# Kernel tuning notes

Measured on AMD Instinct MI355X. Metric: run time of the kernel, lower is better.

## Reference

```python
import jax, jax.numpy as jnp
import numpy as np

PATCH = 14
DIM = 512
LEVELS = 6
ITERS = LEVELS * 2  # default iters
TOKEN_ATTEND_SELF_VALUE = -0.0005


def setup_inputs() -> dict:
    key = jax.random.key(0)
    ks = jax.random.split(key, 9)
    b = 8
    # weights scaled down (~1/sqrt(dim)) so 12 iterations stay finite in fp32
    s = 0.02
    return {
        "img": jax.random.normal(ks[0], (b, 3, 224, 224), jnp.float32),
        "W_patch": jax.random.normal(ks[1], (PATCH * PATCH * 3, DIM), jnp.float32) * s,
        "b_patch": jax.random.normal(ks[2], (DIM,), jnp.float32) * s,
        "pos_emb": jax.random.normal(ks[3], (256, DIM), jnp.float32) * s,
        "init_levels": jax.random.normal(ks[4], (LEVELS, DIM), jnp.float32),
        "bu_in": jax.random.normal(ks[5], (LEVELS - 1, DIM, 4 * DIM), jnp.float32) * s,
        "bu_out": jax.random.normal(ks[6], (LEVELS - 1, 4 * DIM, DIM), jnp.float32) * s,
        "td_in": jax.random.normal(ks[7], (LEVELS - 1, DIM, 4 * DIM), jnp.float32) * s,
        "td_out": jax.random.normal(ks[8], (LEVELS - 1, 4 * DIM, DIM), jnp.float32) * s,
    }


def _grouped_ff(x, w_in, w_out):
    # x: [b, n, groups, d]; per-group two-layer FF with exact GELU
    h = jnp.einsum('bnld,lde->bnle', x, w_in)
    h = jax.nn.gelu(h, approximate=False)
    return jnp.einsum('bnld,lde->bnle', h, w_out)


def _consensus(levels):
    # levels: [b, n, l, d]; attend_self=False, no local radius
    n, d = levels.shape[1], levels.shape[-1]
    norm = jnp.maximum(jnp.linalg.norm(levels, axis=-1, keepdims=True), 1e-12)
    k = levels / norm
    sim = jnp.einsum('bild,bjld->blij', levels, k) * (d ** -0.5)
    eye = jnp.eye(n, dtype=bool)[None, None]
    sim = jnp.where(eye, jnp.asarray(TOKEN_ATTEND_SELF_VALUE, sim.dtype), sim)
    attn = jax.nn.softmax(sim, axis=-1)
    return jnp.einsum('blij,bjld->bild', attn, levels)


def reference(img, W_patch, b_patch, pos_emb, init_levels, bu_in, bu_out, td_in, td_out):
    b, c, H, W = img.shape
    p = PATCH
    h, w = H // p, W // p
    # 'b c (h p1) (w p2) -> b (h w) (p1 p2 c)'
    x = img.reshape(b, c, h, p, w, p).transpose(0, 2, 4, 3, 5, 1).reshape(b, h * w, p * p * c)
    tokens = x @ W_patch + b_patch  # [b, n, d]
    n = tokens.shape[1]
    pos = pos_emb[:n][None, :, None, :]       # [1, n, 1, d]
    bottom = tokens[:, :, None, :]            # [b, n, 1, d]
    levels = jnp.broadcast_to(init_levels[None, None], (b, n, LEVELS, DIM))

    for _ in range(ITERS):
        lwi = jnp.concatenate([bottom, levels], axis=2)            # [b, n, L+1, d]
        bu = _grouped_ff(lwi[:, :, 1:-1], bu_in, bu_out)           # [b, n, L-1, d]
        td = _grouped_ff(lwi[:, :, 2:] + pos, td_in, td_out)       # [b, n, L-1, d]
        bu = jnp.concatenate([bottom, bu], axis=2)                 # [b, n, L, d]
        td = jnp.pad(td, ((0, 0), (0, 0), (0, 1), (0, 0)))         # [b, n, L, d]
        cons = _consensus(levels)
        levels = (levels + bu + td + cons) * 0.25
    return levels
```

## Files before the change

### kernel.cpp

```cpp
#include <hip/hip_runtime.h>
#include <hip/hip_bf16.h>
#include <math.h>

#define B_   8
#define N_   256
#define L_   6
#define D_   512
#define NT_  2048
#define HID_ 2048

typedef __attribute__((ext_vector_type(4))) float f32x4;
typedef __attribute__((ext_vector_type(8))) short bf16x8;

struct bf16x4s { __hip_bfloat16 x, y, z, w; };

__device__ __forceinline__ bf16x4s to_bf4(float a, float b, float c, float d) {
    bf16x4s r;
    r.x = __float2bfloat16(a); r.y = __float2bfloat16(b);
    r.z = __float2bfloat16(c); r.w = __float2bfloat16(d);
    return r;
}

__device__ __forceinline__ void gload16(const void* g, void* l) {
    __builtin_amdgcn_global_load_lds(
        (const __attribute__((address_space(1))) int*)g,
        (__attribute__((address_space(3))) int*)l, 16, 0, 0);
}

template<int BM, int BN, int WM, int WN, typename CT, bool GELU>
__global__ __launch_bounds__(512, 4) void gemm_ff(
    const __hip_bfloat16* __restrict__ A1, int lda1, long az1,
    const __hip_bfloat16* __restrict__ A2, int lda2, long az2, int zsplit,
    const __hip_bfloat16* __restrict__ B, int ldb, long bz,
    CT* __restrict__ C, int ldc, long cz, int K)
{
    constexpr int WVM = BM / WM, WVN = BN / WN;
    constexpr int MR = WVM / 16, NR = WVN / 16;
    constexpr int ALOADS = (BM * 64) / (512 * 8);
    constexpr int BLOADS = (BN * 64) / (512 * 8);
    constexpr int LOADS  = ALOADS + BLOADS;

    __shared__ short As[2][BM * 64];
    __shared__ short Bs[2][BN * 64];

    const int tid = threadIdx.x;
    const int wv = tid >> 6, lane = tid & 63;
    const int wr = wv / WN, wc = wv % WN;

    const int gx = gridDim.x, gy = gridDim.y;
    const int nwg = gx * gy * gridDim.z;
    int lid = (blockIdx.z * gy + blockIdx.y) * gx + blockIdx.x;
    lid = (lid & 7) * (nwg >> 3) + (lid >> 3);
    const int bx = lid % gx, by = (lid / gx) % gy, bzz = lid / (gx * gy);

    const __hip_bfloat16* A;
    int lda;
    if (bzz < zsplit) { A = A1 + (long)bzz * az1;            lda = lda1; }
    else              { A = A2 + (long)(bzz - zsplit) * az2; lda = lda2; }
    B += (long)bzz * bz;  C += (long)bzz * cz;
    const int m0 = by * BM, n0 = bx * BN;

    f32x4 acc[MR][NR] = {};

    const int srow_a = tid >> 3, sslot = tid & 7;

#define STAGE(BUF, K0)                                                        \
    {                                                                         \
        _Pragma("unroll")                                                     \
        for (int i = 0; i < ALOADS; ++i) {                                    \
            const int row = srow_a + i * 64;                                  \
            const int gs  = sslot ^ (row & 7);                                \
            gload16(A + (long)(m0 + row) * lda + (K0) + gs * 8,               \
                    &As[BUF][(wv * 64 + i * 512) * 8]);                       \
        }                                                                     \
        _Pragma("unroll")                                                     \
        for (int i = 0; i < BLOADS; ++i) {                                    \
            const int row = srow_a + i * 64;                                  \
            const int gs  = sslot ^ (row & 7);                                \
            gload16(B + (long)(n0 + row) * ldb + (K0) + gs * 8,               \
                    &Bs[BUF][(wv * 64 + i * 512) * 8]);                       \
        }                                                                     \
    }

    const int fr = lane & 15, k4 = lane >> 4;
    const int nt = K / 64;
    int cur = 0;

    STAGE(0, 0);

    for (int t = 0; t < nt; ++t) {
        if (t + 1 < nt) {
            STAGE(cur ^ 1, (t + 1) * 64);
            asm volatile("s_waitcnt vmcnt(%0)\n\ts_barrier"
                         :: "n"(LOADS) : "memory");
        } else {
            asm volatile("s_waitcnt vmcnt(0)\n\ts_barrier" ::: "memory");
        }

#pragma unroll
        for (int ks = 0; ks < 2; ++ks) {
            bf16x8 af[MR], bf[NR];
#pragma unroll
            for (int i = 0; i < MR; ++i) {
                const int r = wr * WVM + i * 16 + fr;
                af[i] = *(const bf16x8*)&As[cur][r * 64 + ((ks * 4 + k4) ^ (r & 7)) * 8];
            }
#pragma unroll
            for (int j = 0; j < NR; ++j) {
                const int r = wc * WVN + j * 16 + fr;
                bf[j] = *(const bf16x8*)&Bs[cur][r * 64 + ((ks * 4 + k4) ^ (r & 7)) * 8];
            }
            __builtin_amdgcn_s_setprio(1);
#pragma unroll
            for (int i = 0; i < MR; ++i)
#pragma unroll
                for (int j = 0; j < NR; ++j)
                    acc[i][j] = __builtin_amdgcn_mfma_f32_16x16x32_bf16(
                        af[i], bf[j], acc[i][j], 0, 0, 0);
            __builtin_amdgcn_s_setprio(0);
        }
        asm volatile("s_waitcnt lgkmcnt(0)\n\ts_barrier" ::: "memory");
        cur ^= 1;
    }
#undef STAGE

    const int cr4 = (lane >> 4) * 4, cc = lane & 15;
#pragma unroll
    for (int i = 0; i < MR; ++i)
#pragma unroll
        for (int j = 0; j < NR; ++j) {
            const int col = n0 + wc * WVN + j * 16 + cc;
#pragma unroll
            for (int r = 0; r < 4; ++r) {
                const int row = m0 + wr * WVM + i * 16 + cr4 + r;
                float v = acc[i][j][r];
                if (GELU) v = 0.5f * v * (1.0f + erff(v * 0.70710678118654752f));
                CT* p = &C[(long)row * ldc + col];
                if constexpr (sizeof(CT) == 2) *p = __float2bfloat16(v);
                else *p = (CT)v;
            }
        }
}

__device__ __forceinline__ void mfma_kloop(
    const __hip_bfloat16* __restrict__ A, int lda,
    const __hip_bfloat16* __restrict__ B, int ldb,
    int m0, int n0, int K, short* As, short* Bs,
    f32x4 acc[4][4], int wave, int lane)
{
    const int srow_in = lane >> 2;
    const int sslot   = lane & 3;
    const int wm = (wave >> 1) * 64, wn = (wave & 1) * 64;

    for (int k0 = 0; k0 < K; k0 += 32) {
        __syncthreads();
#pragma unroll
        for (int c = 0; c < 2; ++c) {
            const int rbase = c * 64 + wave * 16;
            const int row   = rbase + srow_in;
            const int gk    = sslot ^ ((row >> 1) & 3);
            gload16(A + (long)(m0 + row) * lda + k0 + gk * 8, As + rbase * 32);
            gload16(B + (long)(n0 + row) * ldb + k0 + gk * 8, Bs + rbase * 32);
        }
        __syncthreads();

        const int fr = lane & 15, ksub = lane >> 4;
        bf16x8 af[4], bfr[4];
#pragma unroll
        for (int i = 0; i < 4; ++i) {
            const int ra = wm + i * 16 + fr;
            af[i]  = *(const bf16x8*)(As + ra * 32 + (ksub ^ ((ra >> 1) & 3)) * 8);
            const int rb = wn + i * 16 + fr;
            bfr[i] = *(const bf16x8*)(Bs + rb * 32 + (ksub ^ ((rb >> 1) & 3)) * 8);
        }
#pragma unroll
        for (int i = 0; i < 4; ++i)
#pragma unroll
            for (int j = 0; j < 4; ++j)
                acc[i][j] = __builtin_amdgcn_mfma_f32_16x16x32_bf16(
                    af[i], bfr[j], acc[i][j], 0, 0, 0);
    }
}

template<typename CT, bool GELU>
__global__ __launch_bounds__(256) void gemm_mfma(
    const __hip_bfloat16* __restrict__ A, int lda, long az,
    const __hip_bfloat16* __restrict__ B, int ldb, long bz,
    CT* __restrict__ C, int ldc, long cz, int K,
    const float* __restrict__ bias)
{
    __shared__ short As[128 * 32];
    __shared__ short Bs[128 * 32];
    const int tid = threadIdx.x;
    const int wave = tid >> 6, lane = tid & 63;
    const int z = blockIdx.z;
    A += (long)z * az;  B += (long)z * bz;  C += (long)z * cz;
    const int m0 = blockIdx.y * 128, n0 = blockIdx.x * 128;
    const int wm = (wave >> 1) * 64, wn = (wave & 1) * 64;

    f32x4 acc[4][4] = {};
    mfma_kloop(A, lda, B, ldb, m0, n0, K, As, Bs, acc, wave, lane);

    const int cr = lane >> 4, cc = lane & 15;
#pragma unroll
    for (int j = 0; j < 4; ++j) {
        const int col = n0 + wn + j * 16 + cc;
        const float bv = bias ? bias[col] : 0.f;
#pragma unroll
        for (int i = 0; i < 4; ++i)
#pragma unroll
            for (int r = 0; r < 4; ++r) {
                const int row = m0 + wm + i * 16 + cr * 4 + r;
                float v = acc[i][j][r] + bv;
                if (GELU) v = 0.5f * v * (1.0f + erff(v * 0.70710678118654752f));
                CT* p = &C[(long)row * ldc + col];
                if constexpr (sizeof(CT) == 2) *p = __float2bfloat16(v);
                else *p = (CT)v;
            }
    }
}

__global__ __launch_bounds__(256) void sim_mfma(
    const __hip_bfloat16* __restrict__ lev_bf, const float* __restrict__ invn,
    float* __restrict__ sim)
{
    __shared__ short As[128 * 32];
    __shared__ short Bs[128 * 32];
    const int tid = threadIdx.x;
    const int wave = tid >> 6, lane = tid & 63;
    const int z = blockIdx.z;
    const int b = z / 6, l = z - 6 * b;
    const __hip_bfloat16* base = lev_bf + (long)b * (N_ * L_ * D_) + (long)l * D_;
    const int m0 = blockIdx.y * 128, n0 = blockIdx.x * 128;
    const int wm = (wave >> 1) * 64, wn = (wave & 1) * 64;

    f32x4 acc[4][4] = {};
    mfma_kloop(base, L_ * D_, base, L_ * D_, m0, n0, D_, As, Bs, acc, wave, lane);

    const int cr = lane >> 4, cc = lane & 15;
    const float sc = 0.044194173824159216f;
#pragma unroll
    for (int j = 0; j < 4; ++j) {
        const int jg = n0 + wn + j * 16 + cc;
        const float iv = invn[((long)b * N_ + jg) * L_ + l] * sc;
#pragma unroll
        for (int i = 0; i < 4; ++i)
#pragma unroll
            for (int r = 0; r < 4; ++r) {
                const int ig = m0 + wm + i * 16 + cr * 4 + r;
                float v = acc[i][j][r] * iv;
                if (ig == jg) v = -0.0005f;
                sim[((long)z * N_ + ig) * N_ + jg] = v;
            }
    }
}

__global__ __launch_bounds__(256) void cons_mfma(
    const __hip_bfloat16* __restrict__ attn, const __hip_bfloat16* __restrict__ levT,
    float* __restrict__ cons)
{
    __shared__ short As[128 * 32];
    __shared__ short Bs[128 * 32];
    const int tid = threadIdx.x;
    const int wave = tid >> 6, lane = tid & 63;
    const int z = blockIdx.z;
    const int b = z / 6, l = z - 6 * b;
    const __hip_bfloat16* A = attn + (long)z * N_ * N_;
    const __hip_bfloat16* B = levT + (long)z * D_ * N_;
    float* C = cons + (long)b * (N_ * L_ * D_) + (long)l * D_;
    const int m0 = blockIdx.y * 128, n0 = blockIdx.x * 128;
    const int wm = (wave >> 1) * 64, wn = (wave & 1) * 64;

    f32x4 acc[4][4] = {};
    mfma_kloop(A, N_, B, N_, m0, n0, N_, As, Bs, acc, wave, lane);

    const int cr = lane >> 4, cc = lane & 15;
#pragma unroll
    for (int j = 0; j < 4; ++j) {
        const int col = n0 + wn + j * 16 + cc;
#pragma unroll
        for (int i = 0; i < 4; ++i)
#pragma unroll
            for (int r = 0; r < 4; ++r) {
                const int row = m0 + wm + i * 16 + cr * 4 + r;
                C[(long)row * (L_ * D_) + col] = acc[i][j][r];
            }
    }
}

__global__ __launch_bounds__(256) void transpose_to_bf16(
    const float* __restrict__ src, __hip_bfloat16* __restrict__ dst,
    int R, int Cc)
{
    __shared__ float t[32][33];
    const int zz = blockIdx.z;
    src += (long)zz * R * Cc;  dst += (long)zz * R * Cc;
    const int tx = threadIdx.x & 31, ty = threadIdx.x >> 5;
    const int c0 = blockIdx.x * 32, r0 = blockIdx.y * 32;
#pragma unroll
    for (int i = 0; i < 4; ++i)
        t[ty + i * 8][tx] = src[(long)(r0 + ty + i * 8) * Cc + c0 + tx];
    __syncthreads();
#pragma unroll
    for (int i = 0; i < 4; ++i)
        dst[(long)(c0 + ty + i * 8) * R + r0 + tx] = __float2bfloat16(t[tx][ty + i * 8]);
}

__global__ __launch_bounds__(256) void levT_kernel(
    const float* __restrict__ levels, __hip_bfloat16* __restrict__ levT)
{
    __shared__ float t[32][33];
    const int z = blockIdx.z;
    const int b = z / 6, l = z - 6 * b;
    const float* base = levels + (long)b * (N_ * L_ * D_) + (long)l * D_;
    const int tx = threadIdx.x & 31, ty = threadIdx.x >> 5;
    const int d0 = blockIdx.x * 32, j0 = blockIdx.y * 32;
#pragma unroll
    for (int i = 0; i < 4; ++i)
        t[ty + i * 8][tx] = base[(long)(j0 + ty + i * 8) * (L_ * D_) + d0 + tx];
    __syncthreads();
#pragma unroll
    for (int i = 0; i < 4; ++i)
        levT[(long)z * D_ * N_ + (long)(d0 + ty + i * 8) * N_ + j0 + tx] =
            __float2bfloat16(t[tx][ty + i * 8]);
}

__global__ __launch_bounds__(256) void invnorm_kernel(
    const float* __restrict__ levels, float* __restrict__ invn)
{
    const int wid = blockIdx.x * 4 + (threadIdx.x >> 6);
    const int lane = threadIdx.x & 63;
    const float* row = levels + (long)wid * 512;
    float s = 0.f;
#pragma unroll
    for (int k = lane * 4; k < 512; k += 256) {
        const float4 v = *(const float4*)&row[k];
        s += v.x * v.x + v.y * v.y + v.z * v.z + v.w * v.w;
    }
#pragma unroll
    for (int o = 1; o < 64; o <<= 1) s += __shfl_xor(s, o);
    if (lane == 0) invn[wid] = 1.0f / fmaxf(sqrtf(s), 1e-12f);
}

__global__ __launch_bounds__(256) void softmax_kernel(
    const float* __restrict__ sim, __hip_bfloat16* __restrict__ attn)
{
    const long row = (long)blockIdx.x * 4 + (threadIdx.x >> 6);
    const int lane = threadIdx.x & 63;
    const float* p = sim + row * 256;
    float4 v = *(const float4*)&p[lane * 4];
    float m = fmaxf(fmaxf(v.x, v.y), fmaxf(v.z, v.w));
#pragma unroll
    for (int o = 1; o < 64; o <<= 1) m = fmaxf(m, __shfl_xor(m, o));
    v.x = expf(v.x - m); v.y = expf(v.y - m);
    v.z = expf(v.z - m); v.w = expf(v.w - m);
    float s = v.x + v.y + v.z + v.w;
#pragma unroll
    for (int o = 1; o < 64; o <<= 1) s += __shfl_xor(s, o);
    const float inv = 1.0f / s;
    *(bf16x4s*)&attn[row * 256 + lane * 4] =
        to_bf4(v.x * inv, v.y * inv, v.z * inv, v.w * inv);
}

__global__ __launch_bounds__(256) void patchify_kernel(
    const float* __restrict__ img, __hip_bfloat16* __restrict__ Xp)
{
    const int t = blockIdx.x;
    const int b = t >> 8, n = t & 255;
    const int hh = n >> 4, ww = n & 15;
    for (int k = threadIdx.x; k < 608; k += 256) {
        float v = 0.f;
        if (k < 588) {
            const int c = k % 3;
            const int pj = (k / 3) % 14;
            const int pi = k / 42;
            v = img[(((long)b * 3 + c) * 224 + (hh * 14 + pi)) * 224 + (ww * 14 + pj)];
        }
        Xp[(long)t * 608 + k] = __float2bfloat16(v);
    }
}

__global__ __launch_bounds__(256) void wpT_kernel(
    const float* __restrict__ Wp, __hip_bfloat16* __restrict__ WpT)
{
    __shared__ float t[32][33];
    const int k0 = blockIdx.x * 32, d0 = blockIdx.y * 32;
    const int tx = threadIdx.x & 31, ty = threadIdx.x >> 5;
#pragma unroll
    for (int i = 0; i < 4; ++i) {
        const int k = k0 + ty + i * 8;
        t[ty + i * 8][tx] = (k < 588) ? Wp[(long)k * 512 + d0 + tx] : 0.f;
    }
    __syncthreads();
#pragma unroll
    for (int i = 0; i < 4; ++i)
        WpT[(long)(d0 + ty + i * 8) * 608 + k0 + tx] = __float2bfloat16(t[tx][ty + i * 8]);
}

__global__ __launch_bounds__(256) void init_levels_kernel(
    float* __restrict__ levels, const float* __restrict__ initlv)
{
    const long f = (long)blockIdx.x * 256 + threadIdx.x;
    const int d4 = f & 127;
    const int l = (int)((f >> 7) % 6);
    *(float4*)&levels[f * 4] = *(const float4*)&initlv[(long)l * 512 + d4 * 4];
}

__global__ __launch_bounds__(256) void lev_lp_init(
    const float* __restrict__ levels, const float* __restrict__ pos,
    __hip_bfloat16* __restrict__ lev_bf, __hip_bfloat16* __restrict__ lp_bf)
{
    const long f = (long)blockIdx.x * 256 + threadIdx.x;
    const int d4 = f & 127;
    const long tl = f >> 7;
    const int l = (int)(tl % 6);
    const long t = tl / 6;
    const float4 v = *(const float4*)&levels[f * 4];
    *(bf16x4s*)&lev_bf[f * 4] = to_bf4(v.x, v.y, v.z, v.w);
    if (l >= 1) {
        const float4 p = *(const float4*)&pos[(long)(t & 255) * 512 + d4 * 4];
        *(bf16x4s*)&lp_bf[((t * 5 + l - 1) * 512) + d4 * 4] =
            to_bf4(v.x + p.x, v.y + p.y, v.z + p.z, v.w + p.w);
    }
}

__global__ __launch_bounds__(256) void update_kernel(
    float* __restrict__ levels, const float* __restrict__ tokens,
    const float* __restrict__ acc_bu, const float* __restrict__ acc_td,
    const float* __restrict__ cons, const float* __restrict__ pos,
    __hip_bfloat16* __restrict__ lev_bf, __hip_bfloat16* __restrict__ lp_bf,
    float* __restrict__ invn)
{
    const int wid = blockIdx.x * 4 + (threadIdx.x >> 6);
    const int lane = threadIdx.x & 63;
    const int l = wid % 6;
    const long t = wid / 6;
    const long rowoff = (long)wid * 512;

    float ss = 0.f;
#pragma unroll
    for (int half = 0; half < 2; ++half) {
        const int k = lane * 4 + half * 256;
        const long off = rowoff + k;
        float4 lev = *(const float4*)&levels[off];
        const float4 cns = *(const float4*)&cons[off];
        float4 ac;
        if (l == 0) ac = *(const float4*)&tokens[t * 512 + k];
        else        ac = *(const float4*)&acc_bu[((long)(l - 1) * NT_ + t) * 512 + k];
        if (l < 5) {
            const float4 td = *(const float4*)&acc_td[((long)l * NT_ + t) * 512 + k];
            ac.x += td.x; ac.y += td.y; ac.z += td.z; ac.w += td.w;
        }
        lev.x = (lev.x + ac.x + cns.x) * 0.25f;
        lev.y = (lev.y + ac.y + cns.y) * 0.25f;
        lev.z = (lev.z + ac.z + cns.z) * 0.25f;
        lev.w = (lev.w + ac.w + cns.w) * 0.25f;
        *(float4*)&levels[off] = lev;
        *(bf16x4s*)&lev_bf[off] = to_bf4(lev.x, lev.y, lev.z, lev.w);
        if (l >= 1) {
            const float4 p = *(const float4*)&pos[(long)(t & 255) * 512 + k];
            *(bf16x4s*)&lp_bf[((t * 5 + l - 1) * 512) + k] =
                to_bf4(lev.x + p.x, lev.y + p.y, lev.z + p.z, lev.w + p.w);
        }
        ss += lev.x * lev.x + lev.y * lev.y + lev.z * lev.z + lev.w * lev.w;
    }
#pragma unroll
    for (int o = 1; o < 64; o <<= 1) ss += __shfl_xor(ss, o);
    if (lane == 0) invn[wid] = 1.0f / fmaxf(sqrtf(ss), 1e-12f);
}

extern "C" void kernel_launch(void* const* d_in, const int* in_sizes, int n_in,
                              void* d_out, int out_size, void* d_ws, size_t ws_size,
                              hipStream_t stream)
{
    const float* img    = (const float*)d_in[0];
    const float* Wp     = (const float*)d_in[1];
    const float* bp     = (const float*)d_in[2];
    const float* pos    = (const float*)d_in[3];
    const float* initlv = (const float*)d_in[4];
    const float* bu_in  = (const float*)d_in[5];
    const float* bu_out = (const float*)d_in[6];
    const float* td_in  = (const float*)d_in[7];
    const float* td_out = (const float*)d_in[8];

    float* levels = (float*)d_out;
    float* ws = (float*)d_ws;
    float* tokens  = ws;
    float* acc_bu  = tokens + 1048576;
    float* acc_td  = acc_bu + 5242880;
    __hip_bfloat16* h = (__hip_bfloat16*)(acc_td + 5242880);
    float* invn    = (float*)(h + 41943040);
    __hip_bfloat16* lev_bf   = (__hip_bfloat16*)(invn + 12288);
    __hip_bfloat16* lp_bf    = lev_bf + 6291456;
    __hip_bfloat16* wtin_all = lp_bf + 5242880;
    __hip_bfloat16* wtout_all= wtin_all + 10485760;

    float* sim  = (float*)h;
    float* cons = sim + 3145728;
    __hip_bfloat16* levT_bf = lev_bf;
    __hip_bfloat16* attn_bf = lp_bf;
    __hip_bfloat16* Xp  = (__hip_bfloat16*)acc_bu;
    __hip_bfloat16* WpT = Xp + 1245184;

    init_levels_kernel<<<6144, 256, 0, stream>>>(levels, initlv);
    lev_lp_init<<<6144, 256, 0, stream>>>(levels, pos, lev_bf, lp_bf);
    invnorm_kernel<<<3072, 256, 0, stream>>>(levels, invn);
    patchify_kernel<<<NT_, 256, 0, stream>>>(img, Xp);
    wpT_kernel<<<dim3(19, 16), 256, 0, stream>>>(Wp, WpT);
    gemm_mfma<float, false><<<dim3(4, 16, 1), 256, 0, stream>>>(
        Xp, 608, 0, WpT, 608, 0, tokens, 512, 0, 608, bp);
    transpose_to_bf16<<<dim3(64, 16, 5), 256, 0, stream>>>(bu_in,  wtin_all, 512, 2048);
    transpose_to_bf16<<<dim3(64, 16, 5), 256, 0, stream>>>(td_in,  wtin_all + 5242880, 512, 2048);
    transpose_to_bf16<<<dim3(16, 64, 5), 256, 0, stream>>>(bu_out, wtout_all, 2048, 512);
    transpose_to_bf16<<<dim3(16, 64, 5), 256, 0, stream>>>(td_out, wtout_all + 5242880, 2048, 512);

    for (int it = 0; it < 12; ++it) {
        gemm_ff<128, 128, 2, 4, __hip_bfloat16, true>
            <<<dim3(16, 16, 10), 512, 0, stream>>>(
            lev_bf, L_ * D_, 512,
            lp_bf, 5 * D_, 512, 5,
            wtin_all, D_, (long)HID_ * D_,
            h, HID_, (long)NT_ * HID_, D_);
        gemm_ff<128, 128, 2, 4, float, false>
            <<<dim3(4, 16, 10), 512, 0, stream>>>(
            h, HID_, (long)NT_ * HID_,
            h, HID_, (long)NT_ * HID_, 10,
            wtout_all, HID_, (long)D_ * HID_,
            acc_bu, D_, (long)NT_ * D_, HID_);

        sim_mfma<<<dim3(2, 2, 48), 256, 0, stream>>>(lev_bf, invn, sim);
        softmax_kernel<<<3072, 256, 0, stream>>>(sim, attn_bf);
        levT_kernel<<<dim3(16, 8, 48), 256, 0, stream>>>(levels, levT_bf);
        cons_mfma<<<dim3(4, 2, 48), 256, 0, stream>>>(attn_bf, levT_bf, cons);
        update_kernel<<<3072, 256, 0, stream>>>(levels, tokens, acc_bu, acc_td,
                                                cons, pos, lev_bf, lp_bf, invn);
    }
}
```

Measured before the change: 2.366 ms.

## Use K=32 staging, larger 256x128 tile for FF-in GEMM, and polynomial GELU

```diff
diff --git a/kernel.cpp b/kernel.cpp
--- a/kernel.cpp
+++ b/kernel.cpp
@@ -27,6 +27,20 @@
         (__attribute__((address_space(3))) int*)l, 16, 0, 0);
 }
 
+__device__ __forceinline__ float fast_gelu(float v) {
+    const float x  = v * 0.70710678118654752f;
+    const float ax = fabsf(x);
+    const float t  = __frcp_rn(1.0f + 0.3275911f * ax);
+    float p = fmaf(1.061405429f, t, -1.453152027f);
+    p = fmaf(p, t, 1.421413741f);
+    p = fmaf(p, t, -0.284496736f);
+    p = fmaf(p, t, 0.254829592f);
+    p = p * t;
+    const float e = p * __expf(-ax * ax);
+    const float s = copysignf(1.0f, v);
+    return 0.5f * v * fmaf(s, 1.0f - e, 1.0f);
+}
+
 template<int BM, int BN, int WM, int WN, typename CT, bool GELU>
 __global__ __launch_bounds__(512, 4) void gemm_ff(
     const __hip_bfloat16* __restrict__ A1, int lda1, long az1,
@@ -36,12 +50,12 @@
 {
     constexpr int WVM = BM / WM, WVN = BN / WN;
     constexpr int MR = WVM / 16, NR = WVN / 16;
-    constexpr int ALOADS = (BM * 64) / (512 * 8);
-    constexpr int BLOADS = (BN * 64) / (512 * 8);
+    constexpr int ALOADS = BM / 128;
+    constexpr int BLOADS = BN / 128;
     constexpr int LOADS  = ALOADS + BLOADS;
 
-    __shared__ short As[2][BM * 64];
-    __shared__ short Bs[2][BN * 64];
+    __shared__ short As[2][BM * 32];
+    __shared__ short Bs[2][BN * 32];
 
     const int tid = threadIdx.x;
     const int wv = tid >> 6, lane = tid & 63;
@@ -62,63 +76,61 @@
 
     f32x4 acc[MR][NR] = {};
 
-    const int srow_a = tid >> 3, sslot = tid & 7;
+    const int srow = tid >> 2, sslot = tid & 3;
 
 #define STAGE(BUF, K0)                                                        \
     {                                                                         \
         _Pragma("unroll")                                                     \
         for (int i = 0; i < ALOADS; ++i) {                                    \
-            const int row = srow_a + i * 64;                                  \
-            const int gs  = sslot ^ (row & 7);                                \
+            const int row = srow + i * 128;                                   \
+            const int gs  = sslot ^ ((row >> 1) & 3);                         \
             gload16(A + (long)(m0 + row) * lda + (K0) + gs * 8,               \
-                    &As[BUF][(wv * 64 + i * 512) * 8]);                       \
+                    &As[BUF][i * 4096 + wv * 512]);                           \
         }                                                                     \
         _Pragma("unroll")                                                     \
         for (int i = 0; i < BLOADS; ++i) {                                    \
-            const int row = srow_a + i * 64;                                  \
-            const int gs  = sslot ^ (row & 7);                                \
+            const int row = srow + i * 128;                                   \
+            const int gs  = sslot ^ ((row >> 1) & 3);                         \
             gload16(B + (long)(n0 + row) * ldb + (K0) + gs * 8,               \
-                    &Bs[BUF][(wv * 64 + i * 512) * 8]);                       \
+                    &Bs[BUF][i * 4096 + wv * 512]);                           \
         }                                                                     \
     }
 
     const int fr = lane & 15, k4 = lane >> 4;
-    const int nt = K / 64;
+    const int nt = K / 32;
     int cur = 0;
 
     STAGE(0, 0);
 
     for (int t = 0; t < nt; ++t) {
         if (t + 1 < nt) {
-            STAGE(cur ^ 1, (t + 1) * 64);
+            STAGE(cur ^ 1, (t + 1) * 32);
             asm volatile("s_waitcnt vmcnt(%0)\n\ts_barrier"
                          :: "n"(LOADS) : "memory");
         } else {
             asm volatile("s_waitcnt vmcnt(0)\n\ts_barrier" ::: "memory");
         }
 
-#pragma unroll
-        for (int ks = 0; ks < 2; ++ks) {
-            bf16x8 af[MR], bf[NR];
-#pragma unroll
-            for (int i = 0; i < MR; ++i) {
-                const int r = wr * WVM + i * 16 + fr;
-                af[i] = *(const bf16x8*)&As[cur][r * 64 + ((ks * 4 + k4) ^ (r & 7)) * 8];
-            }
-#pragma unroll
-            for (int j = 0; j < NR; ++j) {
-                const int r = wc * WVN + j * 16 + fr;
-                bf[j] = *(const bf16x8*)&Bs[cur][r * 64 + ((ks * 4 + k4) ^ (r & 7)) * 8];
-            }
-            __builtin_amdgcn_s_setprio(1);
-#pragma unroll
-            for (int i = 0; i < MR; ++i)
-#pragma unroll
-                for (int j = 0; j < NR; ++j)
-                    acc[i][j] = __builtin_amdgcn_mfma_f32_16x16x32_bf16(
-                        af[i], bf[j], acc[i][j], 0, 0, 0);
-            __builtin_amdgcn_s_setprio(0);
-        }
+        bf16x8 af[MR], bf[NR];
+#pragma unroll
+        for (int i = 0; i < MR; ++i) {
+            const int r = wr * WVM + i * 16 + fr;
+            af[i] = *(const bf16x8*)&As[cur][r * 32 + (k4 ^ ((r >> 1) & 3)) * 8];
+        }
+#pragma unroll
+        for (int j = 0; j < NR; ++j) {
+            const int r = wc * WVN + j * 16 + fr;
+            bf[j] = *(const bf16x8*)&Bs[cur][r * 32 + (k4 ^ ((r >> 1) & 3)) * 8];
+        }
+        __builtin_amdgcn_s_setprio(1);
+#pragma unroll
+        for (int i = 0; i < MR; ++i)
+#pragma unroll
+            for (int j = 0; j < NR; ++j)
+                acc[i][j] = __builtin_amdgcn_mfma_f32_16x16x32_bf16(
+                    af[i], bf[j], acc[i][j], 0, 0, 0);
+        __builtin_amdgcn_s_setprio(0);
+
         asm volatile("s_waitcnt lgkmcnt(0)\n\ts_barrier" ::: "memory");
         cur ^= 1;
     }
@@ -134,7 +146,7 @@
             for (int r = 0; r < 4; ++r) {
                 const int row = m0 + wr * WVM + i * 16 + cr4 + r;
                 float v = acc[i][j][r];
-                if (GELU) v = 0.5f * v * (1.0f + erff(v * 0.70710678118654752f));
+                if (GELU) v = fast_gelu(v);
                 CT* p = &C[(long)row * ldc + col];
                 if constexpr (sizeof(CT) == 2) *p = __float2bfloat16(v);
                 else *p = (CT)v;
@@ -212,7 +224,7 @@
             for (int r = 0; r < 4; ++r) {
                 const int row = m0 + wm + i * 16 + cr * 4 + r;
                 float v = acc[i][j][r] + bv;
-                if (GELU) v = 0.5f * v * (1.0f + erff(v * 0.70710678118654752f));
+                if (GELU) v = fast_gelu(v);
                 CT* p = &C[(long)row * ldc + col];
                 if constexpr (sizeof(CT) == 2) *p = __float2bfloat16(v);
                 else *p = (CT)v;
@@ -515,8 +527,8 @@
     transpose_to_bf16<<<dim3(16, 64, 5), 256, 0, stream>>>(td_out, wtout_all + 5242880, 2048, 512);
 
     for (int it = 0; it < 12; ++it) {
-        gemm_ff<128, 128, 2, 4, __hip_bfloat16, true>
-            <<<dim3(16, 16, 10), 512, 0, stream>>>(
+        gemm_ff<256, 128, 4, 2, __hip_bfloat16, true>
+            <<<dim3(16, 8, 10), 512, 0, stream>>>(
             lev_bf, L_ * D_, 512,
             lp_bf, 5 * D_, 512, 5,
             wtin_all, D_, (long)HID_ * D_,
```

Measured after the change: 2.368 ms. No clear change (+0.1%).

## Fuse similarity GEMM with softmax, approximate GELU, store consensus in bf16

Applied to the files above, without the earlier changes.

```diff
diff --git a/kernel.cpp b/kernel.cpp
--- a/kernel.cpp
+++ b/kernel.cpp
@@ -21,10 +21,30 @@
     return r;
 }
 
+__device__ __forceinline__ float bf_to_f(unsigned short u) {
+    union { unsigned int i; float f; } c;
+    c.i = ((unsigned int)u) << 16;
+    return c.f;
+}
+
 __device__ __forceinline__ void gload16(const void* g, void* l) {
     __builtin_amdgcn_global_load_lds(
         (const __attribute__((address_space(1))) int*)g,
         (__attribute__((address_space(3))) int*)l, 16, 0, 0);
+}
+
+__device__ __forceinline__ float fast_gelu(float v) {
+    const float x  = v * 0.70710678118654752f;
+    const float ax = fabsf(x);
+    const float t  = __frcp_rn(1.0f + 0.3275911f * ax);
+    float p = fmaf(1.061405429f, t, -1.453152027f);
+    p = fmaf(p, t, 1.421413741f);
+    p = fmaf(p, t, -0.284496736f);
+    p = fmaf(p, t, 0.254829592f);
+    p = p * t;
+    const float e = p * __expf(-ax * ax);
+    const float s = copysignf(1.0f, v);
+    return 0.5f * v * fmaf(s, 1.0f - e, 1.0f);
 }
 
 template<int BM, int BN, int WM, int WN, typename CT, bool GELU>
@@ -134,11 +154,134 @@
             for (int r = 0; r < 4; ++r) {
                 const int row = m0 + wr * WVM + i * 16 + cr4 + r;
                 float v = acc[i][j][r];
-                if (GELU) v = 0.5f * v * (1.0f + erff(v * 0.70710678118654752f));
+                if (GELU) v = fast_gelu(v);
                 CT* p = &C[(long)row * ldc + col];
                 if constexpr (sizeof(CT) == 2) *p = __float2bfloat16(v);
                 else *p = (CT)v;
             }
+        }
+}
+
+__global__ __launch_bounds__(256) void simsm_kernel(
+    const __hip_bfloat16* __restrict__ lev_bf, const float* __restrict__ invn,
+    __hip_bfloat16* __restrict__ attn)
+{
+    __shared__ short As[64 * 32];
+    __shared__ short Bs[256 * 32];
+    __shared__ float redm[64][4];
+    __shared__ float reds[64][4];
+
+    const int tid = threadIdx.x;
+    const int wv = tid >> 6, lane = tid & 63;
+    const int z = blockIdx.y;
+    const int b = z / 6, l = z - 6 * b;
+    const __hip_bfloat16* base = lev_bf + (long)b * (N_ * L_ * D_) + (long)l * D_;
+    const int m0 = blockIdx.x * 64;
+
+    const int srow = tid >> 2, sslot = tid & 3;
+
+    f32x4 acc[4][4] = {};
+    const int fr = lane & 15, ksub = lane >> 4;
+
+    for (int k0 = 0; k0 < 512; k0 += 32) {
+        __syncthreads();
+        {
+            const int gs = sslot ^ ((srow >> 1) & 3);
+            gload16(base + (long)(m0 + srow) * (L_ * D_) + k0 + gs * 8,
+                    As + wv * 512);
+        }
+#pragma unroll
+        for (int i = 0; i < 4; ++i) {
+            const int row = srow + i * 64;
+            const int gs  = sslot ^ ((row >> 1) & 3);
+            gload16(base + (long)row * (L_ * D_) + k0 + gs * 8,
+                    Bs + i * 2048 + wv * 512);
+        }
+        __syncthreads();
+
+        bf16x8 af[4], bfr[4];
+#pragma unroll
+        for (int i = 0; i < 4; ++i) {
+            const int ra = i * 16 + fr;
+            af[i] = *(const bf16x8*)(As + ra * 32 + (ksub ^ ((ra >> 1) & 3)) * 8);
+            const int rb = wv * 64 + i * 16 + fr;
+            bfr[i] = *(const bf16x8*)(Bs + rb * 32 + (ksub ^ ((rb >> 1) & 3)) * 8);
+        }
+#pragma unroll
+        for (int i = 0; i < 4; ++i)
+#pragma unroll
+            for (int j = 0; j < 4; ++j)
+                acc[i][j] = __builtin_amdgcn_mfma_f32_16x16x32_bf16(
+                    af[i], bfr[j], acc[i][j], 0, 0, 0);
+    }
+
+    const int cr4 = (lane >> 4) * 4, cc = lane & 15;
+    const float sc = 0.044194173824159216f;
+
+    float iv[4];
+#pragma unroll
+    for (int j = 0; j < 4; ++j)
+        iv[j] = invn[((long)b * N_ + wv * 64 + j * 16 + cc) * L_ + l] * sc;
+#pragma unroll
+    for (int i = 0; i < 4; ++i)
+#pragma unroll
+        for (int j = 0; j < 4; ++j) {
+            const int jg = wv * 64 + j * 16 + cc;
+#pragma unroll
+            for (int r = 0; r < 4; ++r) {
+                const int ig = m0 + i * 16 + cr4 + r;
+                float v = acc[i][j][r] * iv[j];
+                if (ig == jg) v = -0.0005f;
+                acc[i][j][r] = v;
+            }
+        }
+
+    __syncthreads();
+
+#pragma unroll
+    for (int i = 0; i < 4; ++i)
+#pragma unroll
+        for (int r = 0; r < 4; ++r) {
+            float m = fmaxf(fmaxf(acc[i][0][r], acc[i][1][r]),
+                            fmaxf(acc[i][2][r], acc[i][3][r]));
+#pragma unroll
+            for (int o = 1; o < 16; o <<= 1) m = fmaxf(m, __shfl_xor(m, o));
+            if (cc == 0) redm[i * 16 + cr4 + r][wv] = m;
+        }
+    __syncthreads();
+
+#pragma unroll
+    for (int i = 0; i < 4; ++i)
+#pragma unroll
+        for (int r = 0; r < 4; ++r) {
+            const int rl = i * 16 + cr4 + r;
+            const float m = fmaxf(fmaxf(redm[rl][0], redm[rl][1]),
+                                  fmaxf(redm[rl][2], redm[rl][3]));
+            float s = 0.f;
+#pragma unroll
+            for (int j = 0; j < 4; ++j) {
+                const float e = expf(acc[i][j][r] - m);
+                acc[i][j][r] = e;
+                s += e;
+            }
+#pragma unroll
+            for (int o = 1; o < 16; o <<= 1) s += __shfl_xor(s, o);
+            if (cc == 0) reds[rl][wv] = s;
+        }
+    __syncthreads();
+
+#pragma unroll
+    for (int i = 0; i < 4; ++i)
+#pragma unroll
+        for (int r = 0; r < 4; ++r) {
+            const int rl = i * 16 + cr4 + r;
+            const float inv = 1.0f / (reds[rl][0] + reds[rl][1] +
+                                      reds[rl][2] + reds[rl][3]);
+            const long rowoff = ((long)z * N_ + m0 + rl) * N_;
+#pragma unroll
+            for (int j = 0; j < 4; ++j)
+                attn[rowoff + wv * 64 + j * 16 + cc] =
+                    __float2bfloat16(acc[i][j][r] * inv);
         }
 }
 
@@ -212,7 +355,7 @@
             for (int r = 0; r < 4; ++r) {
                 const int row = m0 + wm + i * 16 + cr * 4 + r;
                 float v = acc[i][j][r] + bv;
-                if (GELU) v = 0.5f * v * (1.0f + erff(v * 0.70710678118654752f));
+                if (GELU) v = fast_gelu(v);
                 CT* p = &C[(long)row * ldc + col];
                 if constexpr (sizeof(CT) == 2) *p = __float2bfloat16(v);
                 else *p = (CT)v;
@@ -220,44 +363,9 @@
     }
 }
 
-__global__ __launch_bounds__(256) void sim_mfma(
-    const __hip_bfloat16* __restrict__ lev_bf, const float* __restrict__ invn,
-    float* __restrict__ sim)
-{
-    __shared__ short As[128 * 32];
-    __shared__ short Bs[128 * 32];
-    const int tid = threadIdx.x;
-    const int wave = tid >> 6, lane = tid & 63;
-    const int z = blockIdx.z;
-    const int b = z / 6, l = z - 6 * b;
-    const __hip_bfloat16* base = lev_bf + (long)b * (N_ * L_ * D_) + (long)l * D_;
-    const int m0 = blockIdx.y * 128, n0 = blockIdx.x * 128;
-    const int wm = (wave >> 1) * 64, wn = (wave & 1) * 64;
-
-    f32x4 acc[4][4] = {};
-    mfma_kloop(base, L_ * D_, base, L_ * D_, m0, n0, D_, As, Bs, acc, wave, lane);
-
-    const int cr = lane >> 4, cc = lane & 15;
-    const float sc = 0.044194173824159216f;
-#pragma unroll
-    for (int j = 0; j < 4; ++j) {
-        const int jg = n0 + wn + j * 16 + cc;
-        const float iv = invn[((long)b * N_ + jg) * L_ + l] * sc;
-#pragma unroll
-        for (int i = 0; i < 4; ++i)
-#pragma unroll
-            for (int r = 0; r < 4; ++r) {
-                const int ig = m0 + wm + i * 16 + cr * 4 + r;
-                float v = acc[i][j][r] * iv;
-                if (ig == jg) v = -0.0005f;
-                sim[((long)z * N_ + ig) * N_ + jg] = v;
-            }
-    }
-}
-
 __global__ __launch_bounds__(256) void cons_mfma(
     const __hip_bfloat16* __restrict__ attn, const __hip_bfloat16* __restrict__ levT,
-    float* __restrict__ cons)
+    __hip_bfloat16* __restrict__ cons)
 {
     __shared__ short As[128 * 32];
     __shared__ short Bs[128 * 32];
@@ -267,7 +375,7 @@
     const int b = z / 6, l = z - 6 * b;
     const __hip_bfloat16* A = attn + (long)z * N_ * N_;
     const __hip_bfloat16* B = levT + (long)z * D_ * N_;
-    float* C = cons + (long)b * (N_ * L_ * D_) + (long)l * D_;
+    __hip_bfloat16* C = cons + (long)b * (N_ * L_ * D_) + (long)l * D_;
     const int m0 = blockIdx.y * 128, n0 = blockIdx.x * 128;
     const int wm = (wave >> 1) * 64, wn = (wave & 1) * 64;
 
@@ -283,7 +391,7 @@
 #pragma unroll
             for (int r = 0; r < 4; ++r) {
                 const int row = m0 + wm + i * 16 + cr * 4 + r;
-                C[(long)row * (L_ * D_) + col] = acc[i][j][r];
+                C[(long)row * (L_ * D_) + col] = __float2bfloat16(acc[i][j][r]);
             }
     }
 }
@@ -340,26 +448,6 @@
 #pragma unroll
     for (int o = 1; o < 64; o <<= 1) s += __shfl_xor(s, o);
     if (lane == 0) invn[wid] = 1.0f / fmaxf(sqrtf(s), 1e-12f);
-}
-
-__global__ __launch_bounds__(256) void softmax_kernel(
-    const float* __restrict__ sim, __hip_bfloat16* __restrict__ attn)
-{
-    const long row = (long)blockIdx.x * 4 + (threadIdx.x >> 6);
-    const int lane = threadIdx.x & 63;
-    const float* p = sim + row * 256;
-    float4 v = *(const float4*)&p[lane * 4];
-    float m = fmaxf(fmaxf(v.x, v.y), fmaxf(v.z, v.w));
-#pragma unroll
-    for (int o = 1; o < 64; o <<= 1) m = fmaxf(m, __shfl_xor(m, o));
-    v.x = expf(v.x - m); v.y = expf(v.y - m);
-    v.z = expf(v.z - m); v.w = expf(v.w - m);
-    float s = v.x + v.y + v.z + v.w;
-#pragma unroll
-    for (int o = 1; o < 64; o <<= 1) s += __shfl_xor(s, o);
-    const float inv = 1.0f / s;
-    *(bf16x4s*)&attn[row * 256 + lane * 4] =
-        to_bf4(v.x * inv, v.y * inv, v.z * inv, v.w * inv);
 }
 
 __global__ __launch_bounds__(256) void patchify_kernel(
@@ -427,7 +515,7 @@
 __global__ __launch_bounds__(256) void update_kernel(
     float* __restrict__ levels, const float* __restrict__ tokens,
     const float* __restrict__ acc_bu, const float* __restrict__ acc_td,
-    const float* __restrict__ cons, const float* __restrict__ pos,
+    const __hip_bfloat16* __restrict__ cons, const float* __restrict__ pos,
     __hip_bfloat16* __restrict__ lev_bf, __hip_bfloat16* __restrict__ lp_bf,
     float* __restrict__ invn)
 {
@@ -443,7 +531,7 @@
         const int k = lane * 4 + half * 256;
         const long off = rowoff + k;
         float4 lev = *(const float4*)&levels[off];
-        const float4 cns = *(const float4*)&cons[off];
+        const ushort4 cu = *(const ushort4*)&cons[off];
         float4 ac;
         if (l == 0) ac = *(const float4*)&tokens[t * 512 + k];
         else        ac = *(const float4*)&acc_bu[((long)(l - 1) * NT_ + t) * 512 + k];
@@ -451,10 +539,10 @@
             const float4 td = *(const float4*)&acc_td[((long)l * NT_ + t) * 512 + k];
             ac.x += td.x; ac.y += td.y; ac.z += td.z; ac.w += td.w;
         }
-        lev.x = (lev.x + ac.x + cns.x) * 0.25f;
-        lev.y = (lev.y + ac.y + cns.y) * 0.25f;
-        lev.z = (lev.z + ac.z + cns.z) * 0.25f;
-        lev.w = (lev.w + ac.w + cns.w) * 0.25f;
+        lev.x = (lev.x + ac.x + bf_to_f(cu.x)) * 0.25f;
+        lev.y = (lev.y + ac.y + bf_to_f(cu.y)) * 0.25f;
+        lev.z = (lev.z + ac.z + bf_to_f(cu.z)) * 0.25f;
+        lev.w = (lev.w + ac.w + bf_to_f(cu.w)) * 0.25f;
         *(float4*)&levels[off] = lev;
         *(bf16x4s*)&lev_bf[off] = to_bf4(lev.x, lev.y, lev.z, lev.w);
         if (l >= 1) {
@@ -495,8 +583,7 @@
     __hip_bfloat16* wtin_all = lp_bf + 5242880;
     __hip_bfloat16* wtout_all= wtin_all + 10485760;
 
-    float* sim  = (float*)h;
-    float* cons = sim + 3145728;
+    __hip_bfloat16* cons_bf = h;
     __hip_bfloat16* levT_bf = lev_bf;
     __hip_bfloat16* attn_bf = lp_bf;
     __hip_bfloat16* Xp  = (__hip_bfloat16*)acc_bu;
@@ -528,11 +615,10 @@
             wtout_all, HID_, (long)D_ * HID_,
             acc_bu, D_, (long)NT_ * D_, HID_);
 
-        sim_mfma<<<dim3(2, 2, 48), 256, 0, stream>>>(lev_bf, invn, sim);
-        softmax_kernel<<<3072, 256, 0, stream>>>(sim, attn_bf);
+        simsm_kernel<<<dim3(4, 48), 256, 0, stream>>>(lev_bf, invn, attn_bf);
         levT_kernel<<<dim3(16, 8, 48), 256, 0, stream>>>(levels, levT_bf);
-        cons_mfma<<<dim3(4, 2, 48), 256, 0, stream>>>(attn_bf, levT_bf, cons);
+        cons_mfma<<<dim3(4, 2, 48), 256, 0, stream>>>(attn_bf, levT_bf, cons_bf);
         update_kernel<<<3072, 256, 0, stream>>>(levels, tokens, acc_bu, acc_td,
-                                                cons, pos, lev_bf, lp_bf, invn);
-    }
-}
+                                                cons_bf, pos, lev_bf, lp_bf, invn);
+    }
+}
```

After: 2.503 ms. 5.8% more time.
